# Optimization experiments

Hardware: AMD Instinct MI355X
Metric: run time of the kernel (lower is better)

The kernel has to match this reference:

```python
import jax, jax.numpy as jnp
import numpy as np

N_NODES = 50000
N_EDGES = 800000
IN_F = 256
OUT_F = 32
NHEAD = 8
EDGE_F = 32
N_ETYPES = 8
NEG_SLOPE = 0.1


def setup_inputs() -> dict:
    key = jax.random.key(0)
    ks = jax.random.split(key, 10)
    def glorot(k, shape):
        stdv = np.sqrt(6.0 / (shape[-2] + shape[-1]))
        return jax.random.uniform(k, shape, jnp.float32, -stdv, stdv)
    return {
        "x": jax.random.normal(ks[0], (N_NODES, IN_F), jnp.float32),
        "W": glorot(ks[1], (IN_F, OUT_F * NHEAD)),
        "W_e": glorot(ks[2], (EDGE_F, EDGE_F * NHEAD)),
        "edge_emb": glorot(ks[3], (N_ETYPES, EDGE_F)),
        "a_l": glorot(ks[4], (1, NHEAD, OUT_F)),
        "a_r": glorot(ks[5], (1, NHEAD, OUT_F)),
        "a_e": glorot(ks[6], (1, NHEAD, EDGE_F)),
        "row": jax.random.randint(ks[7], (N_EDGES,), 0, N_NODES),
        "col": jax.random.randint(ks[8], (N_EDGES,), 0, N_NODES),
        "tp": jax.random.randint(ks[9], (N_EDGES,), 0, N_ETYPES),
    }


def reference(x, W, W_e, edge_emb, a_l, a_r, a_e, row, col, tp):
    N = x.shape[0]
    H, D = a_l.shape[1], a_l.shape[2]
    # node features -> multi-head; NaN guard as in original
    h = (x @ W).reshape(N, H, D)              # [N, H, D]
    h = jnp.where(jnp.isnan(h), 0.0, h)
    e = (edge_emb @ W_e).reshape(-1, H, EDGE_F)  # [T, H, Fe]
    # per-edge attention logits (gather)
    hl = (a_l * h).sum(-1)                    # [N, H]
    hr = (a_r * h).sum(-1)                    # [N, H]
    he = (a_e * e).sum(-1)                    # [T, H]
    s = hl[row] + hr[col] + he[tp]            # [E, H]
    s = jnp.where(s > 0, s, NEG_SLOPE * s)    # LeakyReLU
    # segment softmax over incoming edges of each destination node (col)
    m = jax.ops.segment_max(s, col, num_segments=N)   # [N, H]
    ex = jnp.exp(s - m[col])                          # [E, H]
    z = jax.ops.segment_sum(ex, col, num_segments=N)  # [N, H]
    att = ex / z[col]                                 # [E, H]
    # multi-head sparse aggregation (mhspmm)
    msg = att[:, :, None] * h[row]                    # [E, H, D]
    out = jax.ops.segment_sum(msg, col, num_segments=N)  # [N, H, D]
    return out.reshape(N, H * D), att
```

## Files before the change

kernel.cpp:

```cpp
#include <hip/hip_runtime.h>
#include <hip/hip_bf16.h>

#define N_NODES 50000
#define N_EDGES 800000
#define IN_F 256
#define OUT_F 32
#define NHEAD 8
#define HD 256
#define EDGE_F 32
#define N_ETYPES 8
#define NEG_SLOPE 0.1f
#define CAP 64
#define ALDS 264

typedef __attribute__((ext_vector_type(8))) short short8;
typedef __attribute__((ext_vector_type(4))) short short4_t;
typedef __attribute__((ext_vector_type(4))) float f32x4;

__device__ __forceinline__ short f2b(float f) {
    __hip_bfloat16 t = __float2bfloat16(f);
    return __builtin_bit_cast(short, t);
}
__device__ __forceinline__ float b2f(short s) {
    return __uint_as_float(((unsigned)(unsigned short)s) << 16);
}

__global__ void prep(const float* __restrict__ W,
                     const float* __restrict__ a_l,
                     const float* __restrict__ a_r,
                     const float* __restrict__ edge_emb,
                     const float* __restrict__ W_e,
                     const float* __restrict__ a_e,
                     __hip_bfloat16* __restrict__ Wt,
                     __hip_bfloat16* __restrict__ Wlr,
                     float* __restrict__ he) {
    int b = blockIdx.x, tid = threadIdx.x;
    if (b < 256) {
        Wt[b * 256 + tid] = __float2bfloat16(W[tid * 256 + b]);
    } else if (b < 272) {
        int idx = (b - 256) * 256 + tid;
        int k = idx >> 4, j = idx & 15;
        const float* av = (j < 8) ? a_l : a_r;
        int hh = j & 7;
        float acc = 0.f;
        #pragma unroll
        for (int d = 0; d < 32; ++d)
            acc += W[k * 256 + hh * 32 + d] * av[hh * 32 + d];
        Wlr[j * 256 + k] = __float2bfloat16(acc);
    } else {
        if (tid < N_ETYPES * NHEAD) {
            int t = tid >> 3, hh = tid & 7;
            float acc = 0.f;
            for (int f = 0; f < EDGE_F; ++f) {
                float ev = 0.f;
                for (int k = 0; k < EDGE_F; ++k)
                    ev += edge_emb[t * EDGE_F + k] * W_e[k * (EDGE_F * NHEAD) + hh * EDGE_F + f];
                acc += a_e[hh * EDGE_F + f] * ev;
            }
            he[t * NHEAD + hh] = acc;
        }
    }
}

__global__ __launch_bounds__(256) void gemm_h_mfma(const float* __restrict__ x,
                                                   const __hip_bfloat16* __restrict__ Wt,
                                                   const __hip_bfloat16* __restrict__ Wlr,
                                                   __hip_bfloat16* __restrict__ h,
                                                   float* __restrict__ hl,
                                                   float* __restrict__ hr) {
    __shared__ short As[64 * ALDS];
    const int tid = threadIdx.x;
    const int wave = tid >> 6;
    const int lane = tid & 63;
    const int row0 = blockIdx.x * 64;
    const int wn0  = wave * 64;
    const int l15  = lane & 15;
    const int kg   = lane >> 4;

    {
        int arow = tid >> 2;
        int kbase = (tid & 3) * 64;
        int grow = row0 + arow;
        const float* xp = &x[(size_t)(grow < N_NODES ? grow : N_NODES - 1) * IN_F + kbase];
        #pragma unroll
        for (int i = 0; i < 8; ++i) {
            float4 lo = *(const float4*)(xp + i * 8);
            float4 hi = *(const float4*)(xp + i * 8 + 4);
            short8 v;
            v[0] = f2b(lo.x); v[1] = f2b(lo.y); v[2] = f2b(lo.z); v[3] = f2b(lo.w);
            v[4] = f2b(hi.x); v[5] = f2b(hi.y); v[6] = f2b(hi.z); v[7] = f2b(hi.w);
            *(short8*)&As[arow * ALDS + kbase + i * 8] = v;
        }
    }
    __syncthreads();

    f32x4 acc[4][4];
    f32x4 accLR[4];
    #pragma unroll
    for (int mi = 0; mi < 4; ++mi) {
        accLR[mi] = (f32x4){0.f, 0.f, 0.f, 0.f};
        #pragma unroll
        for (int ni = 0; ni < 4; ++ni)
            acc[mi][ni] = (f32x4){0.f, 0.f, 0.f, 0.f};
    }

    for (int k0 = 0; k0 < IN_F; k0 += 32) {
        short8 afrag[4];
        #pragma unroll
        for (int mi = 0; mi < 4; ++mi)
            afrag[mi] = *(const short8*)&As[(mi * 16 + l15) * ALDS + k0 + kg * 8];
        short8 bfrag[4];
        #pragma unroll
        for (int ni = 0; ni < 4; ++ni)
            bfrag[ni] = *(const short8*)&Wt[(size_t)(wn0 + ni * 16 + l15) * 256 + k0 + kg * 8];
        #pragma unroll
        for (int mi = 0; mi < 4; ++mi)
            #pragma unroll
            for (int ni = 0; ni < 4; ++ni)
                acc[mi][ni] = __builtin_amdgcn_mfma_f32_16x16x32_bf16(
                    afrag[mi], bfrag[ni], acc[mi][ni], 0, 0, 0);
        if (wave == 0) {
            short8 blr = *(const short8*)&Wlr[(size_t)l15 * 256 + k0 + kg * 8];
            #pragma unroll
            for (int mi = 0; mi < 4; ++mi)
                accLR[mi] = __builtin_amdgcn_mfma_f32_16x16x32_bf16(
                    afrag[mi], blr, accLR[mi], 0, 0, 0);
        }
    }

    #pragma unroll
    for (int mi = 0; mi < 4; ++mi) {
        #pragma unroll
        for (int r = 0; r < 4; ++r) {
            int grow = row0 + mi * 16 + kg * 4 + r;
            if (grow < N_NODES) {
                #pragma unroll
                for (int ni = 0; ni < 4; ++ni) {
                    float v = acc[mi][ni][r];
                    v = (v != v) ? 0.f : v;
                    h[(size_t)grow * HD + wn0 + ni * 16 + l15] = __float2bfloat16(v);
                }
            }
        }
    }
    if (wave == 0) {
        #pragma unroll
        for (int mi = 0; mi < 4; ++mi) {
            #pragma unroll
            for (int r = 0; r < 4; ++r) {
                int grow = row0 + mi * 16 + kg * 4 + r;
                if (grow < N_NODES) {
                    float v = accLR[mi][r];
                    if (l15 < 8) hl[grow * 8 + l15] = v;
                    else         hr[grow * 8 + (l15 - 8)] = v;
                }
            }
        }
    }
}

__global__ void calc_deg(const int* __restrict__ col, int* __restrict__ deg,
                         int* __restrict__ pos) {
    int e = blockIdx.x * 256 + threadIdx.x;
    if (e < N_EDGES) pos[e] = atomicAdd(&deg[col[e]], 1);
}

__global__ void scan1(const int* __restrict__ deg, int* __restrict__ excl,
                      int* __restrict__ bsums, int n) {
    __shared__ int sm[256];
    int tid = threadIdx.x;
    int i = blockIdx.x * 256 + tid;
    int v = (i < n) ? deg[i] : 0;
    sm[tid] = v;
    __syncthreads();
    int acc = v;
    for (int off = 1; off < 256; off <<= 1) {
        int add = (tid >= off) ? sm[tid - off] : 0;
        __syncthreads();
        acc += add;
        sm[tid] = acc;
        __syncthreads();
    }
    if (i < n) excl[i] = acc - v;
    if (tid == 255) bsums[blockIdx.x] = acc;
}

__global__ void scan2(int* __restrict__ bsums, int nb) {
    __shared__ int sm[256];
    int tid = threadIdx.x;
    int v = (tid < nb) ? bsums[tid] : 0;
    sm[tid] = v;
    __syncthreads();
    int acc = v;
    for (int off = 1; off < 256; off <<= 1) {
        int add = (tid >= off) ? sm[tid - off] : 0;
        __syncthreads();
        acc += add;
        sm[tid] = acc;
        __syncthreads();
    }
    if (tid < nb) bsums[tid] = acc - v;
}

__global__ void scan3(int* __restrict__ offs, const int* __restrict__ bsums,
                      int n, int total) {
    int i = blockIdx.x * 256 + threadIdx.x;
    if (i < n) offs[i] += bsums[blockIdx.x];
    if (i == 0) offs[n] = total;
}

__global__ void scatter_edges(const int* __restrict__ col,
                              const int* __restrict__ row,
                              const int* __restrict__ tp,
                              const int* __restrict__ offs,
                              const int* __restrict__ pos,
                              int2* __restrict__ epack) {
    int e = blockIdx.x * 256 + threadIdx.x;
    if (e < N_EDGES) {
        int c = col[e];
        epack[offs[c] + pos[e]] = make_int2(row[e] | (tp[e] << 17), e);
    }
}

__global__ __launch_bounds__(256) void node_fused(const int* __restrict__ offs,
                                                  const int2* __restrict__ epack,
                                                  const float* __restrict__ hl,
                                                  const float* __restrict__ hr,
                                                  const float* __restrict__ he,
                                                  const __hip_bfloat16* __restrict__ h,
                                                  float* __restrict__ out,
                                                  float* __restrict__ att) {
    __shared__ float sc[4][CAP][8];
    int wid = threadIdx.x >> 6;
    int lane = threadIdx.x & 63;
    int n = blockIdx.x * 4 + wid;
    if (n >= N_NODES) return;
    int beg = offs[n], end = offs[n + 1], deg = end - beg;

    int slot = lane >> 3, hh = lane & 7;
    float hrv = hr[n * 8 + hh];
    float m = -1e30f, z = 0.f;
    for (int jj = slot; jj < deg; jj += 8) {
        int2 p = epack[beg + jj];
        int r = p.x & 0x1FFFF, t = p.x >> 17;
        float s = hl[r * 8 + hh] + hrv + he[t * 8 + hh];
        s = s > 0.f ? s : NEG_SLOPE * s;
        if (jj < CAP) sc[wid][jj][hh] = s;
        if (s > m) { z = z * __expf(m - s) + 1.f; m = s; }
        else       { z += __expf(s - m); }
    }
    {
        float mo, zo, M;
        mo = __shfl_xor(m, 8);  zo = __shfl_xor(z, 8);
        M = fmaxf(m, mo); z = z * __expf(m - M) + zo * __expf(mo - M); m = M;
        mo = __shfl_xor(m, 16); zo = __shfl_xor(z, 16);
        M = fmaxf(m, mo); z = z * __expf(m - M) + zo * __expf(mo - M); m = M;
        mo = __shfl_xor(m, 32); zo = __shfl_xor(z, 32);
        M = fmaxf(m, mo); z = z * __expf(m - M) + zo * __expf(mo - M); m = M;
    }
    float zinv = 1.0f / z;

    int hh3 = lane >> 3, dg = lane & 7;
    float m3 = __shfl(m, hh3);
    float zinv3 = __shfl(zinv, hh3);
    float hrv3 = __shfl(hrv, hh3);

    float4 acc = make_float4(0.f, 0.f, 0.f, 0.f);
    int jj = 0;
    for (; jj + 2 <= deg; jj += 2) {
        int2 p0 = epack[beg + jj];
        int2 p1 = epack[beg + jj + 1];
        int r0 = p0.x & 0x1FFFF, r1 = p1.x & 0x1FFFF;
        short4_t hv0 = *(const short4_t*)&h[(size_t)r0 * HD + lane * 4];
        short4_t hv1 = *(const short4_t*)&h[(size_t)r1 * HD + lane * 4];
        float s0, s1;
        if (jj < CAP)     s0 = sc[wid][jj][hh3];
        else { int t = p0.x >> 17; s0 = hl[r0 * 8 + hh3] + hrv3 + he[t * 8 + hh3];
               s0 = s0 > 0.f ? s0 : NEG_SLOPE * s0; }
        if (jj + 1 < CAP) s1 = sc[wid][jj + 1][hh3];
        else { int t = p1.x >> 17; s1 = hl[r1 * 8 + hh3] + hrv3 + he[t * 8 + hh3];
               s1 = s1 > 0.f ? s1 : NEG_SLOPE * s1; }
        float a0 = __expf(s0 - m3) * zinv3;
        float a1 = __expf(s1 - m3) * zinv3;
        if (dg == 0) {
            att[(size_t)p0.y * 8 + hh3] = a0;
            att[(size_t)p1.y * 8 + hh3] = a1;
        }
        acc.x += a0 * b2f(hv0[0]) + a1 * b2f(hv1[0]);
        acc.y += a0 * b2f(hv0[1]) + a1 * b2f(hv1[1]);
        acc.z += a0 * b2f(hv0[2]) + a1 * b2f(hv1[2]);
        acc.w += a0 * b2f(hv0[3]) + a1 * b2f(hv1[3]);
    }
    for (; jj < deg; ++jj) {
        int2 p = epack[beg + jj];
        int r = p.x & 0x1FFFF;
        float s;
        if (jj < CAP) s = sc[wid][jj][hh3];
        else { int t = p.x >> 17; s = hl[r * 8 + hh3] + hrv3 + he[t * 8 + hh3];
               s = s > 0.f ? s : NEG_SLOPE * s; }
        float a = __expf(s - m3) * zinv3;
        if (dg == 0) att[(size_t)p.y * 8 + hh3] = a;
        short4_t hv = *(const short4_t*)&h[(size_t)r * HD + lane * 4];
        acc.x += a * b2f(hv[0]);
        acc.y += a * b2f(hv[1]);
        acc.z += a * b2f(hv[2]);
        acc.w += a * b2f(hv[3]);
    }
    *(float4*)&out[(size_t)n * HD + lane * 4] = acc;
}

extern "C" void kernel_launch(void* const* d_in, const int* in_sizes, int n_in,
                              void* d_out, int out_size, void* d_ws, size_t ws_size,
                              hipStream_t stream) {
    const float* x        = (const float*)d_in[0];
    const float* W        = (const float*)d_in[1];
    const float* W_e      = (const float*)d_in[2];
    const float* edge_emb = (const float*)d_in[3];
    const float* a_l      = (const float*)d_in[4];
    const float* a_r      = (const float*)d_in[5];
    const float* a_e      = (const float*)d_in[6];
    const int*   row      = (const int*)d_in[7];
    const int*   col      = (const int*)d_in[8];
    const int*   tp       = (const int*)d_in[9];

    float* out = (float*)d_out;
    float* att = out + (size_t)N_NODES * HD;

    __hip_bfloat16* h   = (__hip_bfloat16*)d_ws;
    float* hl           = (float*)(h + 12800000);
    float* hr           = hl + 400000;
    float* he           = hr + 400000;
    __hip_bfloat16* Wt  = (__hip_bfloat16*)(he + 64);
    __hip_bfloat16* Wlr = Wt + 65536;
    int*   deg          = (int*)(Wlr + 4096);
    int*   offs         = deg + 50000;
    int*   bsums        = offs + 50001;
    int*   pos          = bsums + 256;
    int*   pad          = pos + 800000;
    int2*  epack        = (int2*)((((uintptr_t)pad) + 7) & ~(uintptr_t)7);

    hipMemsetAsync(deg, 0, (size_t)50000 * 4, stream);

    prep<<<273, 256, 0, stream>>>(W, a_l, a_r, edge_emb, W_e, a_e, Wt, Wlr, he);

    gemm_h_mfma<<<(N_NODES + 63) / 64, 256, 0, stream>>>(x, Wt, Wlr, h, hl, hr);

    const int EB = (N_EDGES + 255) / 256;
    calc_deg<<<EB, 256, 0, stream>>>(col, deg, pos);

    const int NB = (N_NODES + 255) / 256;
    scan1<<<NB, 256, 0, stream>>>(deg, offs, bsums, N_NODES);
    scan2<<<1, 256, 0, stream>>>(bsums, NB);
    scan3<<<NB, 256, 0, stream>>>(offs, bsums, N_NODES, N_EDGES);
    scatter_edges<<<EB, 256, 0, stream>>>(col, row, tp, offs, pos, epack);

    node_fused<<<(N_NODES + 3) / 4, 256, 0, stream>>>(offs, epack, hl, hr, he, h, out, att);
}
```

Before: 326.1 us.

## Fold degree counting into prep kernel and cache edge data in LDS for aggregation

```diff
diff --git a/kernel.cpp b/kernel.cpp
--- a/kernel.cpp
+++ b/kernel.cpp
@@ -31,9 +31,12 @@
                      const float* __restrict__ edge_emb,
                      const float* __restrict__ W_e,
                      const float* __restrict__ a_e,
+                     const int* __restrict__ col,
                      __hip_bfloat16* __restrict__ Wt,
                      __hip_bfloat16* __restrict__ Wlr,
-                     float* __restrict__ he) {
+                     float* __restrict__ he,
+                     int* __restrict__ deg,
+                     int* __restrict__ pos) {
     int b = blockIdx.x, tid = threadIdx.x;
     if (b < 256) {
         Wt[b * 256 + tid] = __float2bfloat16(W[tid * 256 + b]);
@@ -47,7 +50,7 @@
         for (int d = 0; d < 32; ++d)
             acc += W[k * 256 + hh * 32 + d] * av[hh * 32 + d];
         Wlr[j * 256 + k] = __float2bfloat16(acc);
-    } else {
+    } else if (b == 272) {
         if (tid < N_ETYPES * NHEAD) {
             int t = tid >> 3, hh = tid & 7;
             float acc = 0.f;
@@ -59,6 +62,9 @@
             }
             he[t * NHEAD + hh] = acc;
         }
+    } else {
+        int e = (b - 273) * 256 + tid;
+        if (e < N_EDGES) pos[e] = atomicAdd(&deg[col[e]], 1);
     }
 }
 
@@ -157,12 +163,6 @@
             }
         }
     }
-}
-
-__global__ void calc_deg(const int* __restrict__ col, int* __restrict__ deg,
-                         int* __restrict__ pos) {
-    int e = blockIdx.x * 256 + threadIdx.x;
-    if (e < N_EDGES) pos[e] = atomicAdd(&deg[col[e]], 1);
 }
 
 __global__ void scan1(const int* __restrict__ deg, int* __restrict__ excl,
@@ -231,11 +231,14 @@
                                                   float* __restrict__ out,
                                                   float* __restrict__ att) {
     __shared__ float sc[4][CAP][8];
+    __shared__ int   srt[4][CAP];
+    __shared__ int   sei[4][CAP];
     int wid = threadIdx.x >> 6;
     int lane = threadIdx.x & 63;
     int n = blockIdx.x * 4 + wid;
     if (n >= N_NODES) return;
     int beg = offs[n], end = offs[n + 1], deg = end - beg;
+    int cdeg = deg < CAP ? deg : CAP;
 
     int slot = lane >> 3, hh = lane & 7;
     float hrv = hr[n * 8 + hh];
@@ -243,6 +246,7 @@
     for (int jj = slot; jj < deg; jj += 8) {
         int2 p = epack[beg + jj];
         int r = p.x & 0x1FFFF, t = p.x >> 17;
+        if (jj < CAP && hh == 0) { srt[wid][jj] = p.x; sei[wid][jj] = p.y; }
         float s = hl[r * 8 + hh] + hrv + he[t * 8 + hh];
         s = s > 0.f ? s : NEG_SLOPE * s;
         if (jj < CAP) sc[wid][jj][hh] = s;
@@ -260,51 +264,58 @@
     }
     float zinv = 1.0f / z;
 
-    int hh3 = lane >> 3, dg = lane & 7;
-    float m3 = __shfl(m, hh3);
-    float zinv3 = __shfl(zinv, hh3);
-    float hrv3 = __shfl(hrv, hh3);
-
+    for (int jj = slot; jj < cdeg; jj += 8) {
+        float a = __expf(sc[wid][jj][hh] - m) * zinv;
+        sc[wid][jj][hh] = a;
+        att[(size_t)sei[wid][jj] * 8 + hh] = a;
+    }
+
+    int hh3 = lane >> 3;
     float4 acc = make_float4(0.f, 0.f, 0.f, 0.f);
     int jj = 0;
-    for (; jj + 2 <= deg; jj += 2) {
-        int2 p0 = epack[beg + jj];
-        int2 p1 = epack[beg + jj + 1];
-        int r0 = p0.x & 0x1FFFF, r1 = p1.x & 0x1FFFF;
+    for (; jj + 4 <= cdeg; jj += 4) {
+        int r0 = srt[wid][jj]     & 0x1FFFF;
+        int r1 = srt[wid][jj + 1] & 0x1FFFF;
+        int r2 = srt[wid][jj + 2] & 0x1FFFF;
+        int r3 = srt[wid][jj + 3] & 0x1FFFF;
         short4_t hv0 = *(const short4_t*)&h[(size_t)r0 * HD + lane * 4];
         short4_t hv1 = *(const short4_t*)&h[(size_t)r1 * HD + lane * 4];
-        float s0, s1;
-        if (jj < CAP)     s0 = sc[wid][jj][hh3];
-        else { int t = p0.x >> 17; s0 = hl[r0 * 8 + hh3] + hrv3 + he[t * 8 + hh3];
-               s0 = s0 > 0.f ? s0 : NEG_SLOPE * s0; }
-        if (jj + 1 < CAP) s1 = sc[wid][jj + 1][hh3];
-        else { int t = p1.x >> 17; s1 = hl[r1 * 8 + hh3] + hrv3 + he[t * 8 + hh3];
-               s1 = s1 > 0.f ? s1 : NEG_SLOPE * s1; }
-        float a0 = __expf(s0 - m3) * zinv3;
-        float a1 = __expf(s1 - m3) * zinv3;
-        if (dg == 0) {
-            att[(size_t)p0.y * 8 + hh3] = a0;
-            att[(size_t)p1.y * 8 + hh3] = a1;
-        }
-        acc.x += a0 * b2f(hv0[0]) + a1 * b2f(hv1[0]);
-        acc.y += a0 * b2f(hv0[1]) + a1 * b2f(hv1[1]);
-        acc.z += a0 * b2f(hv0[2]) + a1 * b2f(hv1[2]);
-        acc.w += a0 * b2f(hv0[3]) + a1 * b2f(hv1[3]);
-    }
-    for (; jj < deg; ++jj) {
-        int2 p = epack[beg + jj];
-        int r = p.x & 0x1FFFF;
-        float s;
-        if (jj < CAP) s = sc[wid][jj][hh3];
-        else { int t = p.x >> 17; s = hl[r * 8 + hh3] + hrv3 + he[t * 8 + hh3];
-               s = s > 0.f ? s : NEG_SLOPE * s; }
-        float a = __expf(s - m3) * zinv3;
-        if (dg == 0) att[(size_t)p.y * 8 + hh3] = a;
+        short4_t hv2 = *(const short4_t*)&h[(size_t)r2 * HD + lane * 4];
+        short4_t hv3 = *(const short4_t*)&h[(size_t)r3 * HD + lane * 4];
+        float a0 = sc[wid][jj][hh3],     a1 = sc[wid][jj + 1][hh3];
+        float a2 = sc[wid][jj + 2][hh3], a3 = sc[wid][jj + 3][hh3];
+        acc.x += a0 * b2f(hv0[0]) + a1 * b2f(hv1[0]) + a2 * b2f(hv2[0]) + a3 * b2f(hv3[0]);
+        acc.y += a0 * b2f(hv0[1]) + a1 * b2f(hv1[1]) + a2 * b2f(hv2[1]) + a3 * b2f(hv3[1]);
+        acc.z += a0 * b2f(hv0[2]) + a1 * b2f(hv1[2]) + a2 * b2f(hv2[2]) + a3 * b2f(hv3[2]);
+        acc.w += a0 * b2f(hv0[3]) + a1 * b2f(hv1[3]) + a2 * b2f(hv2[3]) + a3 * b2f(hv3[3]);
+    }
+    for (; jj < cdeg; ++jj) {
+        int r = srt[wid][jj] & 0x1FFFF;
+        float a = sc[wid][jj][hh3];
         short4_t hv = *(const short4_t*)&h[(size_t)r * HD + lane * 4];
         acc.x += a * b2f(hv[0]);
         acc.y += a * b2f(hv[1]);
         acc.z += a * b2f(hv[2]);
         acc.w += a * b2f(hv[3]);
+    }
+    if (deg > CAP) {
+        int dg = lane & 7;
+        float m3 = __shfl(m, hh3);
+        float zinv3 = __shfl(zinv, hh3);
+        float hrv3 = __shfl(hrv, hh3);
+        for (jj = CAP; jj < deg; ++jj) {
+            int2 p = epack[beg + jj];
+            int r = p.x & 0x1FFFF, t = p.x >> 17;
+            float s = hl[r * 8 + hh3] + hrv3 + he[t * 8 + hh3];
+            s = s > 0.f ? s : NEG_SLOPE * s;
+            float a = __expf(s - m3) * zinv3;
+            if (dg == 0) att[(size_t)p.y * 8 + hh3] = a;
+            short4_t hv = *(const short4_t*)&h[(size_t)r * HD + lane * 4];
+            acc.x += a * b2f(hv[0]);
+            acc.y += a * b2f(hv[1]);
+            acc.z += a * b2f(hv[2]);
+            acc.w += a * b2f(hv[3]);
+        }
     }
     *(float4*)&out[(size_t)n * HD + lane * 4] = acc;
 }
@@ -341,12 +352,11 @@
 
     hipMemsetAsync(deg, 0, (size_t)50000 * 4, stream);
 
-    prep<<<273, 256, 0, stream>>>(W, a_l, a_r, edge_emb, W_e, a_e, Wt, Wlr, he);
+    const int EB = (N_EDGES + 255) / 256;
+    prep<<<273 + EB, 256, 0, stream>>>(W, a_l, a_r, edge_emb, W_e, a_e, col,
+                                       Wt, Wlr, he, deg, pos);
 
     gemm_h_mfma<<<(N_NODES + 63) / 64, 256, 0, stream>>>(x, Wt, Wlr, h, hl, hr);
-
-    const int EB = (N_EDGES + 255) / 256;
-    calc_deg<<<EB, 256, 0, stream>>>(col, deg, pos);
 
     const int NB = (N_NODES + 255) / 256;
     scan1<<<NB, 256, 0, stream>>>(deg, offs, bsums, N_NODES);
```

Result: faster. 298.7 us (-8.4%).
